# Performance work log

Hardware: AMD Instinct MI355X
Metric: run time of the kernel (lower is better)

## Reference

```python
import jax, jax.numpy as jnp
import numpy as np

N_EMB = 8192
D = 512
BETA = 0.25  # commitment_cost, legacy loss: commit + beta*codebook
EPS = 1e-12  # F.normalize eps


def _l2norm(x):
    n = jnp.sqrt(jnp.sum(x * x, axis=-1, keepdims=True))
    return x / jnp.maximum(n, EPS)


def setup_inputs() -> dict:
    key = jax.random.key(0)
    ks = jax.random.split(key, 6)
    z = jax.random.normal(ks[0], (8, 4096, D), dtype=jnp.float32)
    # frozen codebook, init N(0, D^-0.5)
    embedding = jax.random.normal(ks[1], (N_EMB, D), dtype=jnp.float32) * D ** -0.5
    # embedding_proj: Linear(D, D) default torch init
    lim = 1.0 / np.sqrt(D)
    emb_proj_w = jax.random.uniform(ks[2], (D, D), jnp.float32, -lim, lim)
    emb_proj_b = jax.random.uniform(ks[3], (D,), jnp.float32, -lim, lim)
    # z_proj: identity init, zero bias; perturb slightly to make it non-trivial
    z_proj_w = jnp.eye(D, dtype=jnp.float32) + 0.01 * jax.random.normal(ks[4], (D, D), jnp.float32)
    z_proj_b = jnp.zeros((D,), jnp.float32)
    l2_scale = jnp.asarray(10.0, jnp.float32)
    return {"z": z, "embedding": embedding, "emb_proj_w": emb_proj_w,
            "emb_proj_b": emb_proj_b, "z_proj_w": z_proj_w,
            "z_proj_b": z_proj_b, "l2_scale": l2_scale}


def reference(z, embedding, emb_proj_w, emb_proj_b, z_proj_w, z_proj_b, l2_scale):
    B, T, _ = z.shape
    z_flat = z.reshape(-1, D)                              # [BT, D]
    z_proj = z_flat @ z_proj_w.T + z_proj_b                # [BT, D]
    quant_codebook = embedding @ emb_proj_w.T + emb_proj_b  # [N, D]
    # l2-normalized cosine distances (negated similarity)
    z_n = _l2norm(z_proj)
    c_n = _l2norm(quant_codebook)
    distances = -jnp.einsum('bd,nd->bn', z_n, c_n) * l2_scale  # [BT, N]
    idx = jnp.argmin(distances, axis=1)                    # [BT]
    quantized = quant_codebook[idx].reshape(z.shape)       # [B, T, D]
    commit = jnp.mean((jax.lax.stop_gradient(quantized) - z) ** 2)
    codebook = jnp.mean((quantized - jax.lax.stop_gradient(z)) ** 2)
    vq_loss = commit + BETA * codebook                     # legacy=True
    quantized = z + jax.lax.stop_gradient(quantized - z)   # STE
    return quantized, vq_loss, idx.reshape(B, T)
```

## Files before the change

kernel.cpp:

```cpp
#include <hip/hip_runtime.h>
#include <hip/hip_bf16.h>


#define NQ    32768
#define NEMB  8192
#define DD    512

typedef __attribute__((ext_vector_type(8))) short bf16x8;
typedef __attribute__((ext_vector_type(4))) float f32x4;

__device__ __forceinline__ unsigned short f2bf_rne(float f) {
    unsigned u = __float_as_uint(f);
    unsigned r = u + 0x7FFFu + ((u >> 16) & 1u);
    return (unsigned short)(r >> 16);
}
__device__ __forceinline__ float bf2f(unsigned short b) {
    return __uint_as_float(((unsigned)b) << 16);
}

__device__ __forceinline__ void gload16(const void* g, void* l) {
    __builtin_amdgcn_global_load_lds(
        (const __attribute__((address_space(1))) unsigned int*)g,
        (__attribute__((address_space(3))) unsigned int*)l, 16, 0, 0);
}

__global__ __launch_bounds__(256) void k_qc_gemm(const float* __restrict__ emb,
                                                 const float* __restrict__ W,
                                                 const float* __restrict__ bias,
                                                 float* __restrict__ qc) {
    __shared__ float As[16][132];
    __shared__ float Bs[16][68];
    const int n0 = blockIdx.x * 128;
    const int d0 = blockIdx.y * 64;
    const int t  = threadIdx.x;
    const int tx = t & 15, ty = t >> 4;
    float acc[8][4] = {};
    for (int kb = 0; kb < DD; kb += 16) {
        for (int i = 0; i < 8; ++i) {
            int id = t + i * 256;
            int k = id & 15, m = id >> 4;
            As[k][m] = emb[(size_t)(n0 + m) * DD + kb + k];
        }
        for (int i = 0; i < 4; ++i) {
            int id = t + i * 256;
            int k = id & 15, m = id >> 4;
            Bs[k][m] = W[(size_t)(d0 + m) * DD + kb + k];
        }
        __syncthreads();
        for (int k = 0; k < 16; ++k) {
            float4 a0 = *(const float4*)&As[k][ty * 8];
            float4 a1 = *(const float4*)&As[k][ty * 8 + 4];
            float4 b  = *(const float4*)&Bs[k][tx * 4];
            const float av[8] = {a0.x, a0.y, a0.z, a0.w, a1.x, a1.y, a1.z, a1.w};
            const float bv[4] = {b.x, b.y, b.z, b.w};
            for (int i = 0; i < 8; ++i)
                for (int j = 0; j < 4; ++j) acc[i][j] = fmaf(av[i], bv[j], acc[i][j]);
        }
        __syncthreads();
    }
    float4 bv = *(const float4*)&bias[d0 + tx * 4];
    for (int i = 0; i < 8; ++i) {
        int n = n0 + ty * 8 + i;
        float4 o = {acc[i][0] + bv.x, acc[i][1] + bv.y, acc[i][2] + bv.z, acc[i][3] + bv.w};
        *(float4*)&qc[(size_t)n * DD + d0 + tx * 4] = o;
    }
}

__global__ __launch_bounds__(256) void k_norm(const float* __restrict__ qc,
                                              const float* __restrict__ bz,
                                              float* __restrict__ rnorm,
                                              float* __restrict__ tvec) {
    const int n = blockIdx.x;
    const int t = threadIdx.x;
    float ss = 0.f, tb = 0.f;
    for (int d = t; d < DD; d += 256) {
        float v = qc[(size_t)n * DD + d];
        ss += v * v;
        tb += bz[d] * v;
    }
    for (int off = 32; off; off >>= 1) {
        ss += __shfl_down(ss, off);
        tb += __shfl_down(tb, off);
    }
    __shared__ float s1[4], s2[4];
    int wave = t >> 6, lane = t & 63;
    if (lane == 0) { s1[wave] = ss; s2[wave] = tb; }
    __syncthreads();
    if (t == 0) {
        ss = s1[0] + s1[1] + s1[2] + s1[3];
        tb = s2[0] + s2[1] + s2[2] + s2[3];
        float norm = sqrtf(ss);
        float rn = 1.f / fmaxf(norm, 1e-12f);
        rnorm[n] = rn;
        tvec[n] = tb * rn;
    }
}

__global__ __launch_bounds__(256) void k_e_gemm(const float* __restrict__ qc,
                                                const float* __restrict__ Wz,
                                                const float* __restrict__ rnorm,
                                                unsigned short* __restrict__ ehi,
                                                unsigned short* __restrict__ elo) {
    __shared__ float As[16][132];
    __shared__ float Bs[16][68];
    const int n0 = blockIdx.x * 128;
    const int k0 = blockIdx.y * 64;
    const int t  = threadIdx.x;
    const int tx = t & 15, ty = t >> 4;
    float acc[8][4] = {};
    for (int db = 0; db < DD; db += 16) {
        for (int i = 0; i < 8; ++i) {
            int id = t + i * 256;
            int k = id & 15, m = id >> 4;
            As[k][m] = qc[(size_t)(n0 + m) * DD + db + k];
        }
        for (int i = 0; i < 4; ++i) {
            int id = t + i * 256;
            int kc = id & 63, dk = id >> 6;
            Bs[dk][kc] = Wz[(size_t)(db + dk) * DD + k0 + kc];
        }
        __syncthreads();
        for (int k = 0; k < 16; ++k) {
            float4 a0 = *(const float4*)&As[k][ty * 8];
            float4 a1 = *(const float4*)&As[k][ty * 8 + 4];
            float4 b  = *(const float4*)&Bs[k][tx * 4];
            const float av[8] = {a0.x, a0.y, a0.z, a0.w, a1.x, a1.y, a1.z, a1.w};
            const float bv[4] = {b.x, b.y, b.z, b.w};
            for (int i = 0; i < 8; ++i)
                for (int j = 0; j < 4; ++j) acc[i][j] = fmaf(av[i], bv[j], acc[i][j]);
        }
        __syncthreads();
    }
    for (int i = 0; i < 8; ++i) {
        int n = n0 + ty * 8 + i;
        float rn = rnorm[n];
        ushort4 hv, lv;
        float e0 = acc[i][0] * rn, e1 = acc[i][1] * rn, e2 = acc[i][2] * rn, e3 = acc[i][3] * rn;
        hv.x = f2bf_rne(e0); lv.x = f2bf_rne(e0 - bf2f(hv.x));
        hv.y = f2bf_rne(e1); lv.y = f2bf_rne(e1 - bf2f(hv.y));
        hv.z = f2bf_rne(e2); lv.z = f2bf_rne(e2 - bf2f(hv.z));
        hv.w = f2bf_rne(e3); lv.w = f2bf_rne(e3 - bf2f(hv.w));
        *(ushort4*)&ehi[(size_t)n * DD + k0 + tx * 4] = hv;
        *(ushort4*)&elo[(size_t)n * DD + k0 + tx * 4] = lv;
    }
}

__global__ __launch_bounds__(256) void k_zsplit(const float* __restrict__ z,
                                                unsigned short* __restrict__ zhi,
                                                unsigned short* __restrict__ zlo) {
    const int n4 = (NQ * DD) / 4;
    const float4* z4 = (const float4*)z;
    ushort4* h4 = (ushort4*)zhi;
    ushort4* l4 = (ushort4*)zlo;
    for (int i = blockIdx.x * blockDim.x + threadIdx.x; i < n4; i += gridDim.x * blockDim.x) {
        float4 v = z4[i];
        ushort4 h, l;
        h.x = f2bf_rne(v.x); l.x = f2bf_rne(v.x - bf2f(h.x));
        h.y = f2bf_rne(v.y); l.y = f2bf_rne(v.y - bf2f(h.y));
        h.z = f2bf_rne(v.z); l.z = f2bf_rne(v.z - bf2f(h.z));
        h.w = f2bf_rne(v.w); l.w = f2bf_rne(v.w - bf2f(h.w));
        h4[i] = h;
        l4[i] = l;
    }
}

__global__ __launch_bounds__(256, 3) void k_scores(const unsigned short* __restrict__ Ah,
                                                   const unsigned short* __restrict__ Al,
                                                   const unsigned short* __restrict__ Bh,
                                                   const unsigned short* __restrict__ Bl,
                                                   const float* __restrict__ tvec,
                                                   unsigned long long* __restrict__ table) {
    __shared__ unsigned short sAh[128 * 32];
    __shared__ unsigned short sAl[128 * 32];
    __shared__ unsigned short sBh[128 * 32];
    __shared__ unsigned short sBl[128 * 32];

    const int t    = threadIdx.x;
    const int lane = t & 63;
    const int wave = t >> 6;
    const int wm   = wave >> 1;
    const int wn   = wave & 1;
    const int m0   = blockIdx.y * 128;
    const int n0   = blockIdx.x * 128;

    f32x4 acc[4][4];
    for (int i = 0; i < 4; ++i)
        for (int j = 0; j < 4; ++j) acc[i][j] = (f32x4){0.f, 0.f, 0.f, 0.f};

    const int koff = (((lane >> 4) ^ ((lane >> 1) & 3)) << 3);

    for (int kb = 0; kb < DD; kb += 32) {
        for (int r = 0; r < 2; ++r) {
            const int cbase = r * 256 + wave * 64;
            const int c = cbase + lane;
            const int m = c >> 2;
            const int kg = (c & 3) ^ ((m >> 1) & 3);
            const size_t ga = (size_t)(m0 + m) * DD + kb + kg * 8;
            const size_t gb = (size_t)(n0 + m) * DD + kb + kg * 8;
            gload16(Ah + ga, &sAh[cbase * 8]);
            gload16(Al + ga, &sAl[cbase * 8]);
            gload16(Bh + gb, &sBh[cbase * 8]);
            gload16(Bl + gb, &sBl[cbase * 8]);
        }
        __syncthreads();

        bf16x8 afh[4], afl[4], bfh[4], bfl[4];
        const int ar = wm * 64 + (lane & 15);
        const int br = wn * 64 + (lane & 15);
        for (int i = 0; i < 4; ++i) {
            afh[i] = *(const bf16x8*)&sAh[(ar + i * 16) * 32 + koff];
            afl[i] = *(const bf16x8*)&sAl[(ar + i * 16) * 32 + koff];
            bfh[i] = *(const bf16x8*)&sBh[(br + i * 16) * 32 + koff];
            bfl[i] = *(const bf16x8*)&sBl[(br + i * 16) * 32 + koff];
        }
        for (int i = 0; i < 4; ++i)
            for (int j = 0; j < 4; ++j) {
                acc[i][j] = __builtin_amdgcn_mfma_f32_16x16x32_bf16(afh[i], bfh[j], acc[i][j], 0, 0, 0);
                acc[i][j] = __builtin_amdgcn_mfma_f32_16x16x32_bf16(afh[i], bfl[j], acc[i][j], 0, 0, 0);
                acc[i][j] = __builtin_amdgcn_mfma_f32_16x16x32_bf16(afl[i], bfh[j], acc[i][j], 0, 0, 0);
            }
        __syncthreads();
    }

    const int col = lane & 15;
    const int g   = lane >> 4;
    float tc[4];
    for (int tn = 0; tn < 4; ++tn) tc[tn] = tvec[n0 + wn * 64 + tn * 16 + col];

    for (int tm = 0; tm < 4; ++tm) {
        for (int reg = 0; reg < 4; ++reg) {
            float best = -3.4e38f;
            int   bn   = 0x7FFFFFFF;
            for (int tn = 0; tn < 4; ++tn) {
                float v = acc[tm][tn][reg] + tc[tn];
                int n = n0 + wn * 64 + tn * 16 + col;
                if (v > best || (v == best && n < bn)) { best = v; bn = n; }
            }
            for (int off = 1; off < 16; off <<= 1) {
                float ov = __shfl_xor(best, off);
                int   on = __shfl_xor(bn, off);
                if (ov > best || (ov == best && on < bn)) { best = ov; bn = on; }
            }
            if (col == 0) {
                unsigned u = __float_as_uint(best);
                unsigned key = (u & 0x80000000u) ? ~u : (u | 0x80000000u);
                unsigned long long packed =
                    ((unsigned long long)key << 32) |
                    (unsigned long long)(0xFFFFFFFFu - (unsigned)bn);
                int q = m0 + wm * 64 + tm * 16 + g * 4 + reg;
                atomicMax(&table[q], packed);
            }
        }
    }
}

__global__ __launch_bounds__(128) void k_gather(const unsigned long long* __restrict__ table,
                                                const float* __restrict__ qc,
                                                const float* __restrict__ z,
                                                float* __restrict__ outq,
                                                float* __restrict__ partials,
                                                float* __restrict__ outidx) {
    const int q = blockIdx.x;
    const int t = threadIdx.x;
    unsigned long long p = table[q];
    const int idx = (int)(0xFFFFFFFFu - (unsigned)(p & 0xFFFFFFFFull));
    const float4* src = (const float4*)(qc + (size_t)idx * DD);
    const float4* zs  = (const float4*)(z + (size_t)q * DD);
    float4* dst = (float4*)(outq + (size_t)q * DD);
    float4 a = src[t], b = zs[t];
    dst[t] = a;
    float dx = a.x - b.x, dy = a.y - b.y, dz = a.z - b.z, dw = a.w - b.w;
    float ss = dx * dx + dy * dy + dz * dz + dw * dw;
    for (int off = 32; off; off >>= 1) ss += __shfl_down(ss, off);
    __shared__ float sbuf[2];
    if ((t & 63) == 0) sbuf[t >> 6] = ss;
    __syncthreads();
    if (t == 0) {
        partials[q] = sbuf[0] + sbuf[1];
        outidx[q] = (float)idx;
    }
}

__global__ __launch_bounds__(1024) void k_loss(const float* __restrict__ partials,
                                               float* __restrict__ loss) {
    const int t = threadIdx.x;
    float s = 0.f;
    for (int i = t; i < NQ; i += 1024) s += partials[i];
    for (int off = 32; off; off >>= 1) s += __shfl_down(s, off);
    __shared__ float sbuf[16];
    if ((t & 63) == 0) sbuf[t >> 6] = s;
    __syncthreads();
    if (t == 0) {
        float tot = 0.f;
        for (int w = 0; w < 16; ++w) tot += sbuf[w];
        *loss = tot * (1.25f / 16777216.0f);
    }
}

extern "C" void kernel_launch(void* const* d_in, const int* in_sizes, int n_in,
                              void* d_out, int out_size, void* d_ws, size_t ws_size,
                              hipStream_t stream) {
    (void)in_sizes; (void)n_in; (void)out_size; (void)ws_size;
    const float* z   = (const float*)d_in[0];
    const float* emb = (const float*)d_in[1];
    const float* Wp  = (const float*)d_in[2];
    const float* bp  = (const float*)d_in[3];
    const float* Wz  = (const float*)d_in[4];
    const float* bz  = (const float*)d_in[5];

    float* out = (float*)d_out;
    char* ws = (char*)d_ws;
    float* qc            = (float*)(ws + 0);
    float* rnorm         = (float*)(ws + 16777216);
    float* tvec          = (float*)(ws + 16809984);
    unsigned short* ehi  = (unsigned short*)(ws + 16842752);
    unsigned short* elo  = (unsigned short*)(ws + 25231360);
    unsigned short* zhi  = (unsigned short*)(ws + 33619968);
    unsigned short* zlo  = (unsigned short*)(ws + 67174400);
    unsigned long long* table = (unsigned long long*)(ws + 100728832);
    float* partials      = (float*)(ws + 33619968);

    hipMemsetAsync(table, 0, (size_t)NQ * 8, stream);

    k_qc_gemm<<<dim3(NEMB / 128, DD / 64), 256, 0, stream>>>(emb, Wp, bp, qc);
    k_norm<<<NEMB, 256, 0, stream>>>(qc, bz, rnorm, tvec);
    k_e_gemm<<<dim3(NEMB / 128, DD / 64), 256, 0, stream>>>(qc, Wz, rnorm, ehi, elo);
    k_zsplit<<<4096, 256, 0, stream>>>(z, zhi, zlo);
    k_scores<<<dim3(NEMB / 128, NQ / 128), 256, 0, stream>>>(zhi, zlo, ehi, elo, tvec, table);
    k_gather<<<NQ, 128, 0, stream>>>(table, qc, z,
                                     out,
                                     partials,
                                     out + (size_t)NQ * DD + 1);
    k_loss<<<1, 1024, 0, stream>>>(partials, out + (size_t)NQ * DD);
}
```

Measured before the change: 1.110 ms.

## Move codebook projection GEMMs to split-bf16 MFMA kernels

Replaces the two scalar FP32 SIMT GEMMs (codebook projection and the Wz-folded projection) with MFMA bf16 kernels that use a hi/lo split (three MFMAs per tile) to keep near-FP32 accuracy. New pre-pass kernels split the embedding, Wp and a transposed Wz into bf16 hi/lo pairs, and the first GEMM also emits hi/lo copies of qc for the second. This targets the cost of scalar FMA GEMMs on roughly 8192x512x512 shapes. In exchange it adds extra split passes and uncoalesced scalar epilogue stores, and accuracy depends on the 3-term split.

New measurement: 1.007 ms. 9.3% less time.

```diff
diff --git a/kernel.cpp b/kernel.cpp
--- a/kernel.cpp
+++ b/kernel.cpp
@@ -24,45 +24,203 @@
         (__attribute__((address_space(3))) unsigned int*)l, 16, 0, 0);
 }
 
-__global__ __launch_bounds__(256) void k_qc_gemm(const float* __restrict__ emb,
-                                                 const float* __restrict__ W,
-                                                 const float* __restrict__ bias,
-                                                 float* __restrict__ qc) {
-    __shared__ float As[16][132];
-    __shared__ float Bs[16][68];
-    const int n0 = blockIdx.x * 128;
-    const int d0 = blockIdx.y * 64;
-    const int t  = threadIdx.x;
-    const int tx = t & 15, ty = t >> 4;
-    float acc[8][4] = {};
-    for (int kb = 0; kb < DD; kb += 16) {
-        for (int i = 0; i < 8; ++i) {
-            int id = t + i * 256;
-            int k = id & 15, m = id >> 4;
-            As[k][m] = emb[(size_t)(n0 + m) * DD + kb + k];
-        }
+__global__ __launch_bounds__(256) void k_split(const float* __restrict__ src,
+                                               unsigned short* __restrict__ hi,
+                                               unsigned short* __restrict__ lo,
+                                               int n4) {
+    const float4* s4 = (const float4*)src;
+    ushort4* h4 = (ushort4*)hi;
+    ushort4* l4 = (ushort4*)lo;
+    for (int i = blockIdx.x * blockDim.x + threadIdx.x; i < n4; i += gridDim.x * blockDim.x) {
+        float4 v = s4[i];
+        ushort4 h, l;
+        h.x = f2bf_rne(v.x); l.x = f2bf_rne(v.x - bf2f(h.x));
+        h.y = f2bf_rne(v.y); l.y = f2bf_rne(v.y - bf2f(h.y));
+        h.z = f2bf_rne(v.z); l.z = f2bf_rne(v.z - bf2f(h.z));
+        h.w = f2bf_rne(v.w); l.w = f2bf_rne(v.w - bf2f(h.w));
+        h4[i] = h;
+        l4[i] = l;
+    }
+}
+
+__global__ __launch_bounds__(256) void k_wtsplit(const float* __restrict__ W,
+                                                 unsigned short* __restrict__ thi,
+                                                 unsigned short* __restrict__ tlo) {
+    __shared__ float t[32][33];
+    const int bx = blockIdx.x * 32;
+    const int by = blockIdx.y * 32;
+    const int c = threadIdx.x & 31, r0 = threadIdx.x >> 5;
+    for (int i = 0; i < 4; ++i) {
+        int r = r0 + i * 8;
+        t[r][c] = W[(size_t)(by + r) * DD + bx + c];
+    }
+    __syncthreads();
+    for (int i = 0; i < 4; ++i) {
+        int r = r0 + i * 8;
+        float v = t[c][r];
+        unsigned short h = f2bf_rne(v);
+        thi[(size_t)(bx + r) * DD + by + c] = h;
+        tlo[(size_t)(bx + r) * DD + by + c] = f2bf_rne(v - bf2f(h));
+    }
+}
+
+
+__global__ __launch_bounds__(256, 3) void k_qc_mfma(const unsigned short* __restrict__ Ah,
+                                                    const unsigned short* __restrict__ Al,
+                                                    const unsigned short* __restrict__ Bh,
+                                                    const unsigned short* __restrict__ Bl,
+                                                    const float* __restrict__ bias,
+                                                    float* __restrict__ qc,
+                                                    unsigned short* __restrict__ qhi,
+                                                    unsigned short* __restrict__ qlo) {
+    __shared__ unsigned short sAh[128 * 32];
+    __shared__ unsigned short sAl[128 * 32];
+    __shared__ unsigned short sBh[128 * 32];
+    __shared__ unsigned short sBl[128 * 32];
+
+    const int t    = threadIdx.x;
+    const int lane = t & 63;
+    const int wave = t >> 6;
+    const int wm   = wave >> 1;
+    const int wn   = wave & 1;
+    const int m0   = blockIdx.y * 128;
+    const int n0   = blockIdx.x * 128;
+
+    f32x4 acc[4][4];
+    for (int i = 0; i < 4; ++i)
+        for (int j = 0; j < 4; ++j) acc[i][j] = (f32x4){0.f, 0.f, 0.f, 0.f};
+
+    const int koff = (((lane >> 4) ^ ((lane >> 1) & 3)) << 3);
+
+    for (int kb = 0; kb < DD; kb += 32) {
+        for (int r = 0; r < 2; ++r) {
+            const int cbase = r * 256 + wave * 64;
+            const int c = cbase + lane;
+            const int m = c >> 2;
+            const int kg = (c & 3) ^ ((m >> 1) & 3);
+            const size_t ga = (size_t)(m0 + m) * DD + kb + kg * 8;
+            const size_t gb = (size_t)(n0 + m) * DD + kb + kg * 8;
+            gload16(Ah + ga, &sAh[cbase * 8]);
+            gload16(Al + ga, &sAl[cbase * 8]);
+            gload16(Bh + gb, &sBh[cbase * 8]);
+            gload16(Bl + gb, &sBl[cbase * 8]);
+        }
+        __syncthreads();
+
+        bf16x8 afh[4], afl[4], bfh[4], bfl[4];
+        const int ar = wm * 64 + (lane & 15);
+        const int br = wn * 64 + (lane & 15);
         for (int i = 0; i < 4; ++i) {
-            int id = t + i * 256;
-            int k = id & 15, m = id >> 4;
-            Bs[k][m] = W[(size_t)(d0 + m) * DD + kb + k];
-        }
-        __syncthreads();
-        for (int k = 0; k < 16; ++k) {
-            float4 a0 = *(const float4*)&As[k][ty * 8];
-            float4 a1 = *(const float4*)&As[k][ty * 8 + 4];
-            float4 b  = *(const float4*)&Bs[k][tx * 4];
-            const float av[8] = {a0.x, a0.y, a0.z, a0.w, a1.x, a1.y, a1.z, a1.w};
-            const float bv[4] = {b.x, b.y, b.z, b.w};
-            for (int i = 0; i < 8; ++i)
-                for (int j = 0; j < 4; ++j) acc[i][j] = fmaf(av[i], bv[j], acc[i][j]);
-        }
-        __syncthreads();
-    }
-    float4 bv = *(const float4*)&bias[d0 + tx * 4];
-    for (int i = 0; i < 8; ++i) {
-        int n = n0 + ty * 8 + i;
-        float4 o = {acc[i][0] + bv.x, acc[i][1] + bv.y, acc[i][2] + bv.z, acc[i][3] + bv.w};
-        *(float4*)&qc[(size_t)n * DD + d0 + tx * 4] = o;
+            afh[i] = *(const bf16x8*)&sAh[(ar + i * 16) * 32 + koff];
+            afl[i] = *(const bf16x8*)&sAl[(ar + i * 16) * 32 + koff];
+            bfh[i] = *(const bf16x8*)&sBh[(br + i * 16) * 32 + koff];
+            bfl[i] = *(const bf16x8*)&sBl[(br + i * 16) * 32 + koff];
+        }
+        for (int i = 0; i < 4; ++i)
+            for (int j = 0; j < 4; ++j) {
+                acc[i][j] = __builtin_amdgcn_mfma_f32_16x16x32_bf16(afh[i], bfh[j], acc[i][j], 0, 0, 0);
+                acc[i][j] = __builtin_amdgcn_mfma_f32_16x16x32_bf16(afh[i], bfl[j], acc[i][j], 0, 0, 0);
+                acc[i][j] = __builtin_amdgcn_mfma_f32_16x16x32_bf16(afl[i], bfh[j], acc[i][j], 0, 0, 0);
+            }
+        __syncthreads();
+    }
+
+    const int colb = lane & 15;
+    const int g    = lane >> 4;
+    float bcol[4];
+    for (int tn = 0; tn < 4; ++tn) bcol[tn] = bias[n0 + wn * 64 + tn * 16 + colb];
+    for (int tm = 0; tm < 4; ++tm) {
+        for (int reg = 0; reg < 4; ++reg) {
+            int row = m0 + wm * 64 + tm * 16 + g * 4 + reg;
+            for (int tn = 0; tn < 4; ++tn) {
+                int col = n0 + wn * 64 + tn * 16 + colb;
+                float v = acc[tm][tn][reg] + bcol[tn];
+                size_t o = (size_t)row * DD + col;
+                qc[o] = v;
+                unsigned short h = f2bf_rne(v);
+                qhi[o] = h;
+                qlo[o] = f2bf_rne(v - bf2f(h));
+            }
+        }
+    }
+}
+
+__global__ __launch_bounds__(256, 3) void k_e_mfma(const unsigned short* __restrict__ Ah,
+                                                   const unsigned short* __restrict__ Al,
+                                                   const unsigned short* __restrict__ Bh,
+                                                   const unsigned short* __restrict__ Bl,
+                                                   const float* __restrict__ rnorm,
+                                                   unsigned short* __restrict__ ehi,
+                                                   unsigned short* __restrict__ elo) {
+    __shared__ unsigned short sAh[128 * 32];
+    __shared__ unsigned short sAl[128 * 32];
+    __shared__ unsigned short sBh[128 * 32];
+    __shared__ unsigned short sBl[128 * 32];
+
+    const int t    = threadIdx.x;
+    const int lane = t & 63;
+    const int wave = t >> 6;
+    const int wm   = wave >> 1;
+    const int wn   = wave & 1;
+    const int m0   = blockIdx.y * 128;
+    const int n0   = blockIdx.x * 128;
+
+    f32x4 acc[4][4];
+    for (int i = 0; i < 4; ++i)
+        for (int j = 0; j < 4; ++j) acc[i][j] = (f32x4){0.f, 0.f, 0.f, 0.f};
+
+    const int koff = (((lane >> 4) ^ ((lane >> 1) & 3)) << 3);
+
+    for (int kb = 0; kb < DD; kb += 32) {
+        for (int r = 0; r < 2; ++r) {
+            const int cbase = r * 256 + wave * 64;
+            const int c = cbase + lane;
+            const int m = c >> 2;
+            const int kg = (c & 3) ^ ((m >> 1) & 3);
+            const size_t ga = (size_t)(m0 + m) * DD + kb + kg * 8;
+            const size_t gb = (size_t)(n0 + m) * DD + kb + kg * 8;
+            gload16(Ah + ga, &sAh[cbase * 8]);
+            gload16(Al + ga, &sAl[cbase * 8]);
+            gload16(Bh + gb, &sBh[cbase * 8]);
+            gload16(Bl + gb, &sBl[cbase * 8]);
+        }
+        __syncthreads();
+
+        bf16x8 afh[4], afl[4], bfh[4], bfl[4];
+        const int ar = wm * 64 + (lane & 15);
+        const int br = wn * 64 + (lane & 15);
+        for (int i = 0; i < 4; ++i) {
+            afh[i] = *(const bf16x8*)&sAh[(ar + i * 16) * 32 + koff];
+            afl[i] = *(const bf16x8*)&sAl[(ar + i * 16) * 32 + koff];
+            bfh[i] = *(const bf16x8*)&sBh[(br + i * 16) * 32 + koff];
+            bfl[i] = *(const bf16x8*)&sBl[(br + i * 16) * 32 + koff];
+        }
+        for (int i = 0; i < 4; ++i)
+            for (int j = 0; j < 4; ++j) {
+                acc[i][j] = __builtin_amdgcn_mfma_f32_16x16x32_bf16(afh[i], bfh[j], acc[i][j], 0, 0, 0);
+                acc[i][j] = __builtin_amdgcn_mfma_f32_16x16x32_bf16(afh[i], bfl[j], acc[i][j], 0, 0, 0);
+                acc[i][j] = __builtin_amdgcn_mfma_f32_16x16x32_bf16(afl[i], bfh[j], acc[i][j], 0, 0, 0);
+            }
+        __syncthreads();
+    }
+
+    const int colb = lane & 15;
+    const int g    = lane >> 4;
+    for (int tm = 0; tm < 4; ++tm) {
+        const int rbase = m0 + wm * 64 + tm * 16 + g * 4;
+        float4 rn4 = *(const float4*)&rnorm[rbase];
+        const float rnv[4] = {rn4.x, rn4.y, rn4.z, rn4.w};
+        for (int reg = 0; reg < 4; ++reg) {
+            int row = rbase + reg;
+            for (int tn = 0; tn < 4; ++tn) {
+                int col = n0 + wn * 64 + tn * 16 + colb;
+                float v = acc[tm][tn][reg] * rnv[reg];
+                size_t o = (size_t)row * DD + col;
+                unsigned short h = f2bf_rne(v);
+                ehi[o] = h;
+                elo[o] = f2bf_rne(v - bf2f(h));
+            }
+        }
     }
 }
 
@@ -93,74 +251,6 @@
         float rn = 1.f / fmaxf(norm, 1e-12f);
         rnorm[n] = rn;
         tvec[n] = tb * rn;
-    }
-}
-
-__global__ __launch_bounds__(256) void k_e_gemm(const float* __restrict__ qc,
-                                                const float* __restrict__ Wz,
-                                                const float* __restrict__ rnorm,
-                                                unsigned short* __restrict__ ehi,
-                                                unsigned short* __restrict__ elo) {
-    __shared__ float As[16][132];
-    __shared__ float Bs[16][68];
-    const int n0 = blockIdx.x * 128;
-    const int k0 = blockIdx.y * 64;
-    const int t  = threadIdx.x;
-    const int tx = t & 15, ty = t >> 4;
-    float acc[8][4] = {};
-    for (int db = 0; db < DD; db += 16) {
-        for (int i = 0; i < 8; ++i) {
-            int id = t + i * 256;
-            int k = id & 15, m = id >> 4;
-            As[k][m] = qc[(size_t)(n0 + m) * DD + db + k];
-        }
-        for (int i = 0; i < 4; ++i) {
-            int id = t + i * 256;
-            int kc = id & 63, dk = id >> 6;
-            Bs[dk][kc] = Wz[(size_t)(db + dk) * DD + k0 + kc];
-        }
-        __syncthreads();
-        for (int k = 0; k < 16; ++k) {
-            float4 a0 = *(const float4*)&As[k][ty * 8];
-            float4 a1 = *(const float4*)&As[k][ty * 8 + 4];
-            float4 b  = *(const float4*)&Bs[k][tx * 4];
-            const float av[8] = {a0.x, a0.y, a0.z, a0.w, a1.x, a1.y, a1.z, a1.w};
-            const float bv[4] = {b.x, b.y, b.z, b.w};
-            for (int i = 0; i < 8; ++i)
-                for (int j = 0; j < 4; ++j) acc[i][j] = fmaf(av[i], bv[j], acc[i][j]);
-        }
-        __syncthreads();
-    }
-    for (int i = 0; i < 8; ++i) {
-        int n = n0 + ty * 8 + i;
-        float rn = rnorm[n];
-        ushort4 hv, lv;
-        float e0 = acc[i][0] * rn, e1 = acc[i][1] * rn, e2 = acc[i][2] * rn, e3 = acc[i][3] * rn;
-        hv.x = f2bf_rne(e0); lv.x = f2bf_rne(e0 - bf2f(hv.x));
-        hv.y = f2bf_rne(e1); lv.y = f2bf_rne(e1 - bf2f(hv.y));
-        hv.z = f2bf_rne(e2); lv.z = f2bf_rne(e2 - bf2f(hv.z));
-        hv.w = f2bf_rne(e3); lv.w = f2bf_rne(e3 - bf2f(hv.w));
-        *(ushort4*)&ehi[(size_t)n * DD + k0 + tx * 4] = hv;
-        *(ushort4*)&elo[(size_t)n * DD + k0 + tx * 4] = lv;
-    }
-}
-
-__global__ __launch_bounds__(256) void k_zsplit(const float* __restrict__ z,
-                                                unsigned short* __restrict__ zhi,
-                                                unsigned short* __restrict__ zlo) {
-    const int n4 = (NQ * DD) / 4;
-    const float4* z4 = (const float4*)z;
-    ushort4* h4 = (ushort4*)zhi;
-    ushort4* l4 = (ushort4*)zlo;
-    for (int i = blockIdx.x * blockDim.x + threadIdx.x; i < n4; i += gridDim.x * blockDim.x) {
-        float4 v = z4[i];
-        ushort4 h, l;
-        h.x = f2bf_rne(v.x); l.x = f2bf_rne(v.x - bf2f(h.x));
-        h.y = f2bf_rne(v.y); l.y = f2bf_rne(v.y - bf2f(h.y));
-        h.z = f2bf_rne(v.z); l.z = f2bf_rne(v.z - bf2f(h.z));
-        h.w = f2bf_rne(v.w); l.w = f2bf_rne(v.w - bf2f(h.w));
-        h4[i] = h;
-        l4[i] = l;
     }
 }
 
@@ -318,14 +408,30 @@
     unsigned short* zhi  = (unsigned short*)(ws + 33619968);
     unsigned short* zlo  = (unsigned short*)(ws + 67174400);
     unsigned long long* table = (unsigned long long*)(ws + 100728832);
+
+    unsigned short* embhi = (unsigned short*)(ws + 33619968);
+    unsigned short* emblo = (unsigned short*)(ws + 33619968 + 8388608);
+    unsigned short* qchi  = (unsigned short*)(ws + 33619968 + 16777216);
+    unsigned short* qclo  = (unsigned short*)(ws + 33619968 + 25165824);
+    unsigned short* wphi  = (unsigned short*)(ws + 67174400);
+    unsigned short* wplo  = (unsigned short*)(ws + 67174400 + 524288);
+    unsigned short* wzthi = (unsigned short*)(ws + 67174400 + 1048576);
+    unsigned short* wztlo = (unsigned short*)(ws + 67174400 + 1572864);
     float* partials      = (float*)(ws + 33619968);
 
     hipMemsetAsync(table, 0, (size_t)NQ * 8, stream);
 
-    k_qc_gemm<<<dim3(NEMB / 128, DD / 64), 256, 0, stream>>>(emb, Wp, bp, qc);
+    k_split<<<1024, 256, 0, stream>>>(emb, embhi, emblo, NEMB * DD / 4);
+    k_split<<<256, 256, 0, stream>>>(Wp, wphi, wplo, DD * DD / 4);
+    k_wtsplit<<<dim3(16, 16), 256, 0, stream>>>(Wz, wzthi, wztlo);
+
+    k_qc_mfma<<<dim3(DD / 128, NEMB / 128), 256, 0, stream>>>(embhi, emblo, wphi, wplo,
+                                                              bp, qc, qchi, qclo);
     k_norm<<<NEMB, 256, 0, stream>>>(qc, bz, rnorm, tvec);
-    k_e_gemm<<<dim3(NEMB / 128, DD / 64), 256, 0, stream>>>(qc, Wz, rnorm, ehi, elo);
-    k_zsplit<<<4096, 256, 0, stream>>>(z, zhi, zlo);
+    k_e_mfma<<<dim3(DD / 128, NEMB / 128), 256, 0, stream>>>(qchi, qclo, wzthi, wztlo,
+                                                             rnorm, ehi, elo);
+    k_split<<<4096, 256, 0, stream>>>(z, zhi, zlo, NQ * DD / 4);
+
     k_scores<<<dim3(NEMB / 128, NQ / 128), 256, 0, stream>>>(zhi, zlo, ehi, elo, tvec, table);
     k_gather<<<NQ, 128, 0, stream>>>(table, qc, z,
                                      out,
```
